# Kernel tuning notes

Hardware: AMD Instinct MI355X
Metric: run time of the kernel (lower is better)

## Reference

```python
import jax, jax.numpy as jnp
import numpy as np

N_NODES = 50000
N_EDGES = 800000
D_IN = 128
D_OUT = 128


def setup_inputs() -> dict:
    key = jax.random.key(0)
    ks = jax.random.split(key, 6)
    x = jax.random.normal(ks[0], (N_NODES, D_IN), dtype=jnp.float32)
    edge_src = jax.random.randint(ks[1], (N_EDGES,), 0, N_NODES)
    edge_dst = jax.random.randint(ks[2], (N_EDGES,), 0, N_NODES)
    edge_val = jax.random.uniform(ks[3], (N_EDGES,), dtype=jnp.float32)
    W = jax.random.normal(ks[4], (D_OUT, D_IN), dtype=jnp.float32) / np.sqrt(D_IN)
    b = jax.random.normal(ks[5], (D_OUT,), dtype=jnp.float32) * 0.01
    return {"x": x, "edge_src": edge_src, "edge_dst": edge_dst,
            "edge_val": edge_val, "W": W, "b": b}


def reference(x, edge_src, edge_dst, edge_val, W, b):
    # h = sparse.mm(adj, x): for each edge (dst, src, val): h[dst] += val * x[src]
    msgs = edge_val[:, None] * x[edge_src]            # [E, D_IN]
    h = jax.ops.segment_sum(msgs, edge_dst, num_segments=N_NODES)  # [N, D_IN]
    # nn.Linear: h @ W.T + b, then relu activation
    out = jnp.einsum('nd,od->no', h, W) + b           # [N, D_OUT]
    return jax.nn.relu(out)
```

## Files before the change

### kernel.cpp

```cpp
#include <hip/hip_runtime.h>
#include <hip/hip_bf16.h>

#define N_NODES 50000
#define N_EDGES 800000
#define D 128
#define CAP 64
#define EPT 4
#define BUCKET_NB 782

static_assert(N_NODES < 65536, "src must fit in 16 bits for epack");
static_assert(BUCKET_NB * 256 * EPT >= N_EDGES, "bucket grid covers all edges");

typedef __attribute__((ext_vector_type(8))) short short8;
typedef __attribute__((ext_vector_type(4))) float f32x4;
typedef unsigned int uint;
typedef unsigned short ushort;

__device__ __forceinline__ ushort f2bf(float f) {
    uint u = __float_as_uint(f);
    u += 0x7fffu + ((u >> 16) & 1u);
    return (ushort)(u >> 16);
}

__device__ __forceinline__ float bflo(uint u) { return __uint_as_float(u << 16); }
__device__ __forceinline__ float bfhi(uint u) { return __uint_as_float(u & 0xffff0000u); }


__global__ __launch_bounds__(256) void sgcn_gemm_y(
    const float* __restrict__ x, const float* __restrict__ W,
    ushort* __restrict__ y, int* __restrict__ deg)
{
    {
        int t = blockIdx.x * 256 + threadIdx.x;
        if (t * 4 < N_NODES) {
            int4 z = make_int4(0, 0, 0, 0);
            int rem = N_NODES - t * 4;
            if (rem >= 4) reinterpret_cast<int4*>(deg)[t] = z;
            else for (int i = 0; i < rem; ++i) deg[t * 4 + i] = 0;
        }
    }

    int wave = threadIdx.x >> 6;
    int lane = threadIdx.x & 63;
    int lm = lane & 15;
    int kb = lane >> 4;

    short8 bfr[8][4];
#pragma unroll
    for (int nt = 0; nt < 8; ++nt)
#pragma unroll
        for (int kk = 0; kk < 4; ++kk) {
            const float* wp = W + (nt * 16 + lm) * D + kk * 32 + kb * 8;
            float4 a = *reinterpret_cast<const float4*>(wp);
            float4 c = *reinterpret_cast<const float4*>(wp + 4);
            short8 s;
            s[0] = (short)f2bf(a.x); s[1] = (short)f2bf(a.y);
            s[2] = (short)f2bf(a.z); s[3] = (short)f2bf(a.w);
            s[4] = (short)f2bf(c.x); s[5] = (short)f2bf(c.y);
            s[6] = (short)f2bf(c.z); s[7] = (short)f2bf(c.w);
            bfr[nt][kk] = s;
        }

    const int nMT = N_NODES / 16;
    int mt0 = blockIdx.x * 4 + wave;
    int strideMT = gridDim.x * 4;
    for (int mt = mt0; mt < nMT; mt += strideMT) {
        int m0 = mt * 16;
        const float* xrow = x + (long)(m0 + lm) * D + kb * 8;
        short8 afr[4];
#pragma unroll
        for (int kk = 0; kk < 4; ++kk) {
            float4 a = *reinterpret_cast<const float4*>(xrow + kk * 32);
            float4 c = *reinterpret_cast<const float4*>(xrow + kk * 32 + 4);
            short8 s;
            s[0] = (short)f2bf(a.x); s[1] = (short)f2bf(a.y);
            s[2] = (short)f2bf(a.z); s[3] = (short)f2bf(a.w);
            s[4] = (short)f2bf(c.x); s[5] = (short)f2bf(c.y);
            s[6] = (short)f2bf(c.z); s[7] = (short)f2bf(c.w);
            afr[kk] = s;
        }
#pragma unroll
        for (int nt = 0; nt < 8; ++nt) {
            f32x4 acc = {0.f, 0.f, 0.f, 0.f};
#pragma unroll
            for (int kk = 0; kk < 4; ++kk)
                acc = __builtin_amdgcn_mfma_f32_16x16x32_bf16(afr[kk], bfr[nt][kk], acc, 0, 0, 0);
            ushort* yp = y + (long)(m0 + kb * 4) * D + nt * 16 + lm;
#pragma unroll
            for (int r = 0; r < 4; ++r)
                yp[(long)r * D] = f2bf(acc[r]);
        }
    }
}


__global__ __launch_bounds__(256) void sgcn_bucket(
    const int* __restrict__ src, const int* __restrict__ dst,
    const float* __restrict__ val, int* __restrict__ deg,
    uint* __restrict__ epack)
{
    int t = blockIdx.x * 256 + threadIdx.x;
    const int T = BUCKET_NB * 256;

    int  d[EPT], s[EPT], r[EPT];
    float v[EPT];
    bool ok[EPT];
#pragma unroll
    for (int i = 0; i < EPT; ++i) {
        int e = t + i * T;
        ok[i] = e < N_EDGES;
        if (ok[i]) { d[i] = dst[e]; s[i] = src[e]; v[i] = val[e]; }
    }
#pragma unroll
    for (int i = 0; i < EPT; ++i)
        if (ok[i]) r[i] = atomicAdd(&deg[d[i]], 1);
#pragma unroll
    for (int i = 0; i < EPT; ++i)
        if (ok[i] && r[i] < CAP)
            epack[(size_t)d[i] * CAP + r[i]] = ((uint)f2bf(v[i]) << 16) | (uint)s[i];
}


__global__ __launch_bounds__(256) void sgcn_aggregate(
    const uint* __restrict__ yb, const int* __restrict__ deg,
    const uint* __restrict__ ep, const float* __restrict__ bias,
    float* __restrict__ out)
{
    int n = (blockIdx.x * 256 + threadIdx.x) >> 4;
    int c = threadIdx.x & 15;
    float4 bv0 = *reinterpret_cast<const float4*>(bias + c * 8);
    float4 bv1 = *reinterpret_cast<const float4*>(bias + c * 8 + 4);

    int dn = deg[n]; if (dn > CAP) dn = CAP;
    int j0 = n * CAP, j1 = j0 + dn;
    float a0 = 0.f, a1 = 0.f, a2 = 0.f, a3 = 0.f;
    float a4 = 0.f, a5 = 0.f, a6 = 0.f, a7 = 0.f;
    int j = j0;
    for (; j + 4 <= j1; j += 4) {
        uint p0 = __builtin_nontemporal_load(ep + j);
        uint p1 = __builtin_nontemporal_load(ep + j + 1);
        uint p2 = __builtin_nontemporal_load(ep + j + 2);
        uint p3 = __builtin_nontemporal_load(ep + j + 3);
        uint4 u0 = *reinterpret_cast<const uint4*>(yb + (size_t)(p0 & 0xffffu) * 64 + c * 4);
        uint4 u1 = *reinterpret_cast<const uint4*>(yb + (size_t)(p1 & 0xffffu) * 64 + c * 4);
        uint4 u2 = *reinterpret_cast<const uint4*>(yb + (size_t)(p2 & 0xffffu) * 64 + c * 4);
        uint4 u3 = *reinterpret_cast<const uint4*>(yb + (size_t)(p3 & 0xffffu) * 64 + c * 4);
        float v0 = __uint_as_float(p0 & 0xffff0000u);
        float v1 = __uint_as_float(p1 & 0xffff0000u);
        float v2 = __uint_as_float(p2 & 0xffff0000u);
        float v3 = __uint_as_float(p3 & 0xffff0000u);
        a0 += v0 * bflo(u0.x) + v1 * bflo(u1.x) + v2 * bflo(u2.x) + v3 * bflo(u3.x);
        a1 += v0 * bfhi(u0.x) + v1 * bfhi(u1.x) + v2 * bfhi(u2.x) + v3 * bfhi(u3.x);
        a2 += v0 * bflo(u0.y) + v1 * bflo(u1.y) + v2 * bflo(u2.y) + v3 * bflo(u3.y);
        a3 += v0 * bfhi(u0.y) + v1 * bfhi(u1.y) + v2 * bfhi(u2.y) + v3 * bfhi(u3.y);
        a4 += v0 * bflo(u0.z) + v1 * bflo(u1.z) + v2 * bflo(u2.z) + v3 * bflo(u3.z);
        a5 += v0 * bfhi(u0.z) + v1 * bfhi(u1.z) + v2 * bfhi(u2.z) + v3 * bfhi(u3.z);
        a6 += v0 * bflo(u0.w) + v1 * bflo(u1.w) + v2 * bflo(u2.w) + v3 * bflo(u3.w);
        a7 += v0 * bfhi(u0.w) + v1 * bfhi(u1.w) + v2 * bfhi(u2.w) + v3 * bfhi(u3.w);
    }
    for (; j < j1; ++j) {
        uint p = __builtin_nontemporal_load(ep + j);
        uint4 u = *reinterpret_cast<const uint4*>(yb + (size_t)(p & 0xffffu) * 64 + c * 4);
        float v = __uint_as_float(p & 0xffff0000u);
        a0 += v * bflo(u.x); a1 += v * bfhi(u.x);
        a2 += v * bflo(u.y); a3 += v * bfhi(u.y);
        a4 += v * bflo(u.z); a5 += v * bfhi(u.z);
        a6 += v * bflo(u.w); a7 += v * bfhi(u.w);
    }
    f32x4 r0, r1;
    r0[0] = fmaxf(a0 + bv0.x, 0.f);
    r0[1] = fmaxf(a1 + bv0.y, 0.f);
    r0[2] = fmaxf(a2 + bv0.z, 0.f);
    r0[3] = fmaxf(a3 + bv0.w, 0.f);
    r1[0] = fmaxf(a4 + bv1.x, 0.f);
    r1[1] = fmaxf(a5 + bv1.y, 0.f);
    r1[2] = fmaxf(a6 + bv1.z, 0.f);
    r1[3] = fmaxf(a7 + bv1.w, 0.f);
    f32x4* op = reinterpret_cast<f32x4*>(out + (long)n * D + c * 8);
    __builtin_nontemporal_store(r0, op);
    __builtin_nontemporal_store(r1, op + 1);
}

extern "C" void kernel_launch(void* const* d_in, const int* in_sizes, int n_in,
                              void* d_out, int out_size, void* d_ws, size_t ws_size,
                              hipStream_t stream) {
    const float* x   = (const float*)d_in[0];
    const int*   es  = (const int*)d_in[1];
    const int*   ed  = (const int*)d_in[2];
    const float* ev  = (const float*)d_in[3];
    const float* W   = (const float*)d_in[4];
    const float* b   = (const float*)d_in[5];
    float* out = (float*)d_out;

    char* ws = (char*)d_ws;
    size_t off = 0;
    uint* yb    = (uint*)(ws + off); off += (size_t)N_NODES * (D / 2) * sizeof(uint);
    uint* epack = (uint*)(ws + off); off += (size_t)N_NODES * CAP * sizeof(uint);
    int*  deg   = (int*) (ws + off); off += (size_t)N_NODES * sizeof(int);

    sgcn_gemm_y<<<512, 256, 0, stream>>>(x, W, (ushort*)yb, deg);
    sgcn_bucket<<<BUCKET_NB, 256, 0, stream>>>(es, ed, ev, deg, epack);
    sgcn_aggregate<<<3125, 256, 0, stream>>>(yb, deg, epack, b, out);
}
```

Before: 114.0 us.

## Split aggregate feature dimension into quarters across blocks, raise bucket edges per thread

The aggregation kernel now maps 4 threads per node, each handling a 32-channel quarter selected by blockIdx, so consecutive blocks cover the same nodes' different column slices. This makes a wave touch 16 nodes per edge step instead of 4, and it uses cached instead of nontemporal index loads. The goal is more memory-level parallelism and better L2 reuse of the edge lists, which are now read four times. The unroll drops from 4 to 2. The bucket kernel also processes 16 edges per thread with fewer blocks, trading parallelism for more atomics in flight per thread.

```diff
diff --git a/kernel.cpp b/kernel.cpp
--- a/kernel.cpp
+++ b/kernel.cpp
@@ -5,8 +5,8 @@
 #define N_EDGES 800000
 #define D 128
 #define CAP 64
-#define EPT 4
-#define BUCKET_NB 782
+#define EPT 16
+#define BUCKET_NB 196
 
 static_assert(N_NODES < 65536, "src must fit in 16 bits for epack");
 static_assert(BUCKET_NB * 256 * EPT >= N_EDGES, "bucket grid covers all edges");
@@ -121,46 +121,48 @@
 }
 
 
+#define AGG_BPQ 782
+
 __global__ __launch_bounds__(256) void sgcn_aggregate(
     const uint* __restrict__ yb, const int* __restrict__ deg,
     const uint* __restrict__ ep, const float* __restrict__ bias,
     float* __restrict__ out)
 {
-    int n = (blockIdx.x * 256 + threadIdx.x) >> 4;
-    int c = threadIdx.x & 15;
-    float4 bv0 = *reinterpret_cast<const float4*>(bias + c * 8);
-    float4 bv1 = *reinterpret_cast<const float4*>(bias + c * 8 + 4);
+    int q  = blockIdx.x & 3;
+    int nb = blockIdx.x >> 2;
+    int n  = nb * 64 + (threadIdx.x >> 2);
+    if (n >= N_NODES) return;
+    int c4 = threadIdx.x & 3;
+    int ch = q * 32 + c4 * 8;
+    int yo = q * 16 + c4 * 4;
+
+    float4 bv0 = *reinterpret_cast<const float4*>(bias + ch);
+    float4 bv1 = *reinterpret_cast<const float4*>(bias + ch + 4);
 
     int dn = deg[n]; if (dn > CAP) dn = CAP;
     int j0 = n * CAP, j1 = j0 + dn;
     float a0 = 0.f, a1 = 0.f, a2 = 0.f, a3 = 0.f;
     float a4 = 0.f, a5 = 0.f, a6 = 0.f, a7 = 0.f;
     int j = j0;
-    for (; j + 4 <= j1; j += 4) {
-        uint p0 = __builtin_nontemporal_load(ep + j);
-        uint p1 = __builtin_nontemporal_load(ep + j + 1);
-        uint p2 = __builtin_nontemporal_load(ep + j + 2);
-        uint p3 = __builtin_nontemporal_load(ep + j + 3);
-        uint4 u0 = *reinterpret_cast<const uint4*>(yb + (size_t)(p0 & 0xffffu) * 64 + c * 4);
-        uint4 u1 = *reinterpret_cast<const uint4*>(yb + (size_t)(p1 & 0xffffu) * 64 + c * 4);
-        uint4 u2 = *reinterpret_cast<const uint4*>(yb + (size_t)(p2 & 0xffffu) * 64 + c * 4);
-        uint4 u3 = *reinterpret_cast<const uint4*>(yb + (size_t)(p3 & 0xffffu) * 64 + c * 4);
+    for (; j + 2 <= j1; j += 2) {
+        uint p0 = ep[j];
+        uint p1 = ep[j + 1];
+        uint4 u0 = *reinterpret_cast<const uint4*>(yb + (size_t)(p0 & 0xffffu) * 64 + yo);
+        uint4 u1 = *reinterpret_cast<const uint4*>(yb + (size_t)(p1 & 0xffffu) * 64 + yo);
         float v0 = __uint_as_float(p0 & 0xffff0000u);
         float v1 = __uint_as_float(p1 & 0xffff0000u);
-        float v2 = __uint_as_float(p2 & 0xffff0000u);
-        float v3 = __uint_as_float(p3 & 0xffff0000u);
-        a0 += v0 * bflo(u0.x) + v1 * bflo(u1.x) + v2 * bflo(u2.x) + v3 * bflo(u3.x);
-        a1 += v0 * bfhi(u0.x) + v1 * bfhi(u1.x) + v2 * bfhi(u2.x) + v3 * bfhi(u3.x);
-        a2 += v0 * bflo(u0.y) + v1 * bflo(u1.y) + v2 * bflo(u2.y) + v3 * bflo(u3.y);
-        a3 += v0 * bfhi(u0.y) + v1 * bfhi(u1.y) + v2 * bfhi(u2.y) + v3 * bfhi(u3.y);
-        a4 += v0 * bflo(u0.z) + v1 * bflo(u1.z) + v2 * bflo(u2.z) + v3 * bflo(u3.z);
-        a5 += v0 * bfhi(u0.z) + v1 * bfhi(u1.z) + v2 * bfhi(u2.z) + v3 * bfhi(u3.z);
-        a6 += v0 * bflo(u0.w) + v1 * bflo(u1.w) + v2 * bflo(u2.w) + v3 * bflo(u3.w);
-        a7 += v0 * bfhi(u0.w) + v1 * bfhi(u1.w) + v2 * bfhi(u2.w) + v3 * bfhi(u3.w);
-    }
-    for (; j < j1; ++j) {
-        uint p = __builtin_nontemporal_load(ep + j);
-        uint4 u = *reinterpret_cast<const uint4*>(yb + (size_t)(p & 0xffffu) * 64 + c * 4);
+        a0 += v0 * bflo(u0.x) + v1 * bflo(u1.x);
+        a1 += v0 * bfhi(u0.x) + v1 * bfhi(u1.x);
+        a2 += v0 * bflo(u0.y) + v1 * bflo(u1.y);
+        a3 += v0 * bfhi(u0.y) + v1 * bfhi(u1.y);
+        a4 += v0 * bflo(u0.z) + v1 * bflo(u1.z);
+        a5 += v0 * bfhi(u0.z) + v1 * bfhi(u1.z);
+        a6 += v0 * bflo(u0.w) + v1 * bflo(u1.w);
+        a7 += v0 * bfhi(u0.w) + v1 * bfhi(u1.w);
+    }
+    if (j < j1) {
+        uint p = ep[j];
+        uint4 u = *reinterpret_cast<const uint4*>(yb + (size_t)(p & 0xffffu) * 64 + yo);
         float v = __uint_as_float(p & 0xffff0000u);
         a0 += v * bflo(u.x); a1 += v * bfhi(u.x);
         a2 += v * bflo(u.y); a3 += v * bfhi(u.y);
@@ -176,7 +178,7 @@
     r1[1] = fmaxf(a5 + bv1.y, 0.f);
     r1[2] = fmaxf(a6 + bv1.z, 0.f);
     r1[3] = fmaxf(a7 + bv1.w, 0.f);
-    f32x4* op = reinterpret_cast<f32x4*>(out + (long)n * D + c * 8);
+    f32x4* op = reinterpret_cast<f32x4*>(out + (long)n * D + ch);
     __builtin_nontemporal_store(r0, op);
     __builtin_nontemporal_store(r1, op + 1);
 }
@@ -200,5 +202,5 @@
 
     sgcn_gemm_y<<<512, 256, 0, stream>>>(x, W, (ushort*)yb, deg);
     sgcn_bucket<<<BUCKET_NB, 256, 0, stream>>>(es, ed, ev, deg, epack);
-    sgcn_aggregate<<<3125, 256, 0, stream>>>(yb, deg, epack, b, out);
-}
+    sgcn_aggregate<<<AGG_BPQ * 4, 256, 0, stream>>>(yb, deg, epack, b, out);
+}
```

After: 131.3 us. +15.2%, slower.
